# Optimization experiments

Hardware: AMD Instinct MI355X
Metric: run time of the kernel (lower is better)

Reference implementation:

```python
import jax, jax.numpy as jnp
import numpy as np

NS = 50000   # source nodes
NT = 50000   # target nodes
E = 500000   # edges per relation
H = 128      # hidden_channels
SF, TF, ED, OUT = 64, 48, 32, 2


def setup_inputs() -> dict:
    key = jax.random.key(0)
    ks = jax.random.split(key, 40)
    n = lambda i, shape, s=1.0: jax.random.normal(ks[i], shape, jnp.float32) * s
    W = 0.05  # weight scale
    inp = {
        'x_source': n(0, (NS, SF)),
        'x_target': n(1, (NT, TF)),
        'edge_attr_st': n(2, (E, ED)),
        'enc_s_w1': n(3, (H, SF), W), 'enc_s_b1': n(4, (H,), W),
        'enc_s_w2': n(5, (H, H), W), 'enc_s_b2': n(6, (H,), W),
        'enc_t_w1': n(7, (H, TF), W), 'enc_t_b1': n(8, (H,), W),
        'enc_t_w2': n(9, (H, H), W), 'enc_t_b2': n(10, (H,), W),
        'conv_wl': n(11, (3, 4, H, H), W),
        'conv_bl': n(12, (3, 4, H), W),
        'conv_wr': n(13, (3, 4, H, H), W),
        'gate_w1': n(14, (H, 2 * H), W), 'gate_b1': n(15, (H,), W),
        'gate_w2': n(16, (1, H), W), 'gate_b2': n(17, (1,), W),
        'mlp_w1': n(18, (H, H + ED), W), 'mlp_b1': n(19, (H,), W),
        'mlp_w2': n(20, (H // 2, H), W), 'mlp_b2': n(21, (H // 2,), W),
        'mlp_w3': n(22, (OUT, H // 2), W), 'mlp_b3': n(23, (OUT,), W),
        'ei_ss': jax.random.randint(ks[24], (2, E), 0, NS),
        'ei_tt': jax.random.randint(ks[25], (2, E), 0, NT),
        'ei_st': jax.random.randint(ks[26], (2, E), 0, NS),  # row<NS, col<NT (equal here)
        'ei_ts': jax.random.randint(ks[27], (2, E), 0, NT),
    }
    return inp


def _sage(x_src, x_dst, ei, wl, bl, wr, n_dst):
    # PyG SAGEConv(mean): lin_l(scatter_mean(x_src[row] -> col)) + lin_r(x_dst)
    row, col = ei[0], ei[1]
    msg = x_src[row]                                            # [E, H]
    s = jax.ops.segment_sum(msg, col, num_segments=n_dst)      # [n_dst, H]
    cnt = jax.ops.segment_sum(jnp.ones((ei.shape[1],), x_src.dtype), col,
                              num_segments=n_dst)
    agg = s / jnp.maximum(cnt, 1.0)[:, None]
    return agg @ wl.T + bl + x_dst @ wr.T


def reference(x_source, x_target, edge_attr_st,
              enc_s_w1, enc_s_b1, enc_s_w2, enc_s_b2,
              enc_t_w1, enc_t_b1, enc_t_w2, enc_t_b2,
              conv_wl, conv_bl, conv_wr,
              gate_w1, gate_b1, gate_w2, gate_b2,
              mlp_w1, mlp_b1, mlp_w2, mlp_b2, mlp_w3, mlp_b3,
              ei_ss, ei_tt, ei_st, ei_ts):
    relu = jax.nn.relu
    # node encoders (dropout is identity in eval)
    xs = relu(x_source @ enc_s_w1.T + enc_s_b1) @ enc_s_w2.T + enc_s_b2
    xt = relu(x_target @ enc_t_w1.T + enc_t_b1) @ enc_t_w2.T + enc_t_b2

    def hetero_layer(hs, ht, l):
        # relation order: 0=ss, 1=tt, 2=st, 3=ts
        o_ss = _sage(hs, hs, ei_ss, conv_wl[l, 0], conv_bl[l, 0], conv_wr[l, 0], NS)
        o_tt = _sage(ht, ht, ei_tt, conv_wl[l, 1], conv_bl[l, 1], conv_wr[l, 1], NT)
        o_st = _sage(hs, ht, ei_st, conv_wl[l, 2], conv_bl[l, 2], conv_wr[l, 2], NT)
        o_ts = _sage(ht, hs, ei_ts, conv_wl[l, 3], conv_bl[l, 3], conv_wr[l, 3], NS)
        # HeteroConv aggr='mean' over relations per destination node type
        return (o_ss + o_ts) * 0.5, (o_tt + o_st) * 0.5

    h1s, h1t = hetero_layer(xs, xt, 0)
    h1s, h1t = relu(h1s), relu(h1t)
    h2s, h2t = hetero_layer(h1s, h1t, 1)
    h2s, h2t = relu(h2s + h1s), relu(h2t + h1t)
    h3s, h3t = hetero_layer(h2s, h2t, 2)
    h3s, h3t = relu(h3s + h2s), relu(h3t + h2t)

    # edge head on ('source','to','target') — first non-empty relation
    row, col = ei_st[0], ei_st[1]
    src_h = h3s[row]                                            # [E, H]
    tgt_h = h3t[col]                                            # [E, H]
    cat = jnp.concatenate([src_h, tgt_h], axis=1)               # [E, 2H]
    gate = jax.nn.sigmoid(relu(cat @ gate_w1.T + gate_b1) @ gate_w2.T + gate_b2)
    combined = src_h * gate + tgt_h * (1.0 - gate)
    feat = jnp.concatenate([combined, edge_attr_st], axis=1)    # [E, H+ED]
    h = relu(feat @ mlp_w1.T + mlp_b1)
    h = relu(h @ mlp_w2.T + mlp_b2)
    return h @ mlp_w3.T + mlp_b3                                # [E, OUT]
```

## Files before the change

kernel.cpp:

```cpp
#include <hip/hip_runtime.h>
#include <cmath>

#define NSN 50000
#define NTN 50000
#define EE  500000
#define NBE ((size_t)NSN * 128)
#define NPASS 4
#define PRNG 12500

using short8 = __attribute__((ext_vector_type(8))) short;
using f32x4  = __attribute__((ext_vector_type(4))) float;
#define MFMA16(a, b, c) __builtin_amdgcn_mfma_f32_16x16x32_bf16(a, b, c, 0, 0, 0)

__device__ __forceinline__ float  b2f(ushort u) { return __uint_as_float(((uint)u) << 16); }
__device__ __forceinline__ ushort f2b(float f) {
  uint x = __float_as_uint(f);
  uint r = x + 0x7FFFu + ((x >> 16) & 1u);
  return (ushort)(r >> 16);
}
__device__ __forceinline__ float blo(uint x) { return __uint_as_float(x << 16); }
__device__ __forceinline__ float bhi(uint x) { return __uint_as_float(x & 0xFFFF0000u); }
__device__ __forceinline__ uint  pk2(float a, float b) { return (uint)f2b(a) | ((uint)f2b(b) << 16); }

__global__ void cvtall_k(const float* __restrict__ xs, const float* __restrict__ xt,
                         const float* __restrict__ wl,
                         const float* __restrict__ esw1, const float* __restrict__ esw2,
                         const float* __restrict__ etw1, const float* __restrict__ etw2,
                         ushort* __restrict__ xsB, ushort* __restrict__ xtB,
                         ushort* __restrict__ wlB, ushort* __restrict__ esw1B,
                         ushort* __restrict__ esw2B, ushort* __restrict__ etw1B,
                         ushort* __restrict__ etw2B) {
  int i = blockIdx.x * 256 + threadIdx.x;
  if (i < 3200000) { xsB[i] = f2b(xs[i]); return; }
  i -= 3200000;
  if (i < 3200000) {
    int r = i >> 6, k = i & 63;
    xtB[i] = (k < 48) ? f2b(xt[(size_t)r * 48 + k]) : (ushort)0;
    return;
  }
  i -= 3200000;
  if (i < 196608) { wlB[i] = f2b(wl[i]); return; }
  i -= 196608;
  if (i < 8192) { esw1B[i] = f2b(esw1[i]); return; }
  i -= 8192;
  if (i < 16384) { esw2B[i] = f2b(esw2[i]); return; }
  i -= 16384;
  if (i < 8192) {
    int r = i >> 6, k = i & 63;
    etw1B[i] = (k < 48) ? f2b(etw1[(size_t)r * 48 + k]) : (ushort)0;
    return;
  }
  i -= 8192;
  if (i < 16384) { etw2B[i] = f2b(etw2[i]); return; }
}

__global__ void wrc_k(const float* __restrict__ wr, const float* __restrict__ bl,
                      ushort* __restrict__ wrcB, float* __restrict__ blc) {
  int z = blockIdx.y;
  int l = z >> 1, dd = z & 1;
  int r1 = dd ? 1 : 0, r2 = dd ? 2 : 3;
  int idx = blockIdx.x * 256 + threadIdx.x;
  if (idx < 16384) {
    wrcB[(size_t)z * 16384 + idx] =
        f2b(wr[(size_t)(l * 4 + r1) * 16384 + idx] + wr[(size_t)(l * 4 + r2) * 16384 + idx]);
    if (idx < 128)
      blc[z * 128 + idx] = bl[(l * 4 + r1) * 128 + idx] + bl[(l * 4 + r2) * 128 + idx];
  }
}

__global__ void headw_k(const float* __restrict__ gw1, const float* __restrict__ mw1,
                        const float* __restrict__ mw2, const float* __restrict__ gb1,
                        const float* __restrict__ mb1,
                        ushort* __restrict__ Whead, float* __restrict__ biasHead,
                        ushort* __restrict__ w1eB, ushort* __restrict__ w2B) {
  int idx = blockIdx.x * 256 + threadIdx.x;
  if (idx < 65536) {
    int z = idx >> 15, rr = (idx >> 7) & 255, c = idx & 127;
    float v = (rr < 128) ? gw1[(size_t)rr * 256 + z * 128 + c]
                         : mw1[(size_t)(rr - 128) * 160 + c];
    Whead[idx] = f2b(v);
  } else if (idx < 69632) {
    int i = idx - 65536;
    w1eB[i] = f2b(mw1[(size_t)(i >> 5) * 160 + 128 + (i & 31)]);
  } else if (idx < 77824) {
    int i = idx - 69632;
    w2B[i] = f2b(mw2[i]);
  } else if (idx < 78336) {
    int i = idx - 77824;
    int z = i >> 8, n = i & 255;
    biasHead[i] = (n < 128) ? (z ? 0.f : gb1[n]) : mb1[n - 128];
  }
}

__global__ void count4_k(const int* __restrict__ e0, const int* __restrict__ e1,
                         const int* __restrict__ e2, const int* __restrict__ e3,
                         int* __restrict__ cnt) {
  int rel = blockIdx.y;
  const int* col = (rel == 0 ? e0 : rel == 1 ? e1 : rel == 2 ? e2 : e3) + EE;
  int i = blockIdx.x * 256 + threadIdx.x;
  if (i < EE) atomicAdd(&cnt[rel * 50000 + col[i]], 1);
}

__global__ __launch_bounds__(256) void scanA_k(const int* __restrict__ cnt,
                                               int* __restrict__ loc,
                                               int* __restrict__ bsum) {
  __shared__ int ws[4];
  int rel = blockIdx.y, b = blockIdx.x, t = threadIdx.x;
  const int* c = cnt + (size_t)rel * 50000;
  int base = b * 2048 + t * 8;
  int v[8], s = 0;
  #pragma unroll
  for (int i = 0; i < 8; ++i) {
    int idx = base + i;
    v[i] = (idx < 50000) ? c[idx] : 0;
    s += v[i];
  }
  int lane = t & 63, w = t >> 6;
  int x = s;
  #pragma unroll
  for (int d = 1; d < 64; d <<= 1) {
    int y = __shfl_up(x, d, 64);
    if (lane >= d) x += y;
  }
  if (lane == 63) ws[w] = x;
  __syncthreads();
  int add = 0;
  for (int ww = 0; ww < w; ++ww) add += ws[ww];
  int run = add + x - s;
  #pragma unroll
  for (int i = 0; i < 8; ++i) {
    int idx = base + i;
    run += v[i];
    if (idx < 50000) loc[(size_t)rel * 50000 + idx] = run;
  }
  if (t == 255) bsum[rel * 25 + b] = add + x;
}
__global__ void scanB_k(int* __restrict__ bsum) {
  int t = threadIdx.x;
  if (t < 4) {
    int s = 0;
    for (int b = 0; b < 25; ++b) {
      int v = bsum[t * 25 + b];
      bsum[t * 25 + b] = s;
      s += v;
    }
  }
}
__global__ void scanC_k(const int* __restrict__ cnt, int* __restrict__ loc,
                        const int* __restrict__ bsum, int* __restrict__ off,
                        int* __restrict__ cur) {
  int rel = blockIdx.y;
  int i = blockIdx.x * 256 + threadIdx.x;
  if (i < 50000) {
    int incl = loc[(size_t)rel * 50000 + i] + bsum[rel * 25 + i / 2048];
    off[(size_t)rel * 50001 + i + 1] = incl;
    cur[(size_t)rel * 50000 + i] = incl - cnt[(size_t)rel * 50000 + i];
    if (i == 0) off[(size_t)rel * 50001] = 0;
  }
}

__global__ void fillP_k(const int* __restrict__ e0, const int* __restrict__ e1,
                        const int* __restrict__ e2, const int* __restrict__ e3,
                        int* __restrict__ cur, int* __restrict__ adj,
                        int* __restrict__ adjE, int pass) {
  int rel = blockIdx.y;
  const int* ei = rel == 0 ? e0 : rel == 1 ? e1 : rel == 2 ? e2 : e3;
  int e = blockIdx.x * 256 + threadIdx.x;
  if (e < EE) {
    int c = ei[EE + e];
    if (c >= pass * PRNG && c < (pass + 1) * PRNG) {
      int pos = atomicAdd(&cur[rel * 50000 + c], 1);
      adj[(size_t)rel * EE + pos] = ei[e];
      if (rel == 2) adjE[pos] = e;
    }
  }
}

__global__ void colof_k(const int* __restrict__ off, int* __restrict__ colOf, int N) {
  int n = blockIdx.x * 256 + threadIdx.x;
  if (n < N) {
    int s = off[n], e = off[n + 1];
    for (int i = s; i < e; ++i) colOf[i] = n;
  }
}

__global__ void eaperm_k(const float* __restrict__ ea, const int* __restrict__ adjE,
                         ushort* __restrict__ eaB, int E) {
  int idx = blockIdx.x * 256 + threadIdx.x;
  int pos = idx >> 3, q = idx & 7;
  if (pos < E) {
    int eid = adjE[pos];
    float4 v = *(const float4*)(ea + (size_t)eid * 32 + q * 4);
    ushort4 o;
    o.x = f2b(v.x); o.y = f2b(v.y); o.z = f2b(v.z); o.w = f2b(v.w);
    *(ushort4*)(eaB + (size_t)pos * 32 + q * 4) = o;
  }
}

__global__ __launch_bounds__(256) void gather4_k(
    const ushort* __restrict__ hs, const ushort* __restrict__ ht,
    const int* __restrict__ off4, const int* __restrict__ adj4,
    ushort* __restrict__ m0, ushort* __restrict__ m1,
    ushort* __restrict__ m2, ushort* __restrict__ m3, int N) {
  int r = blockIdx.y;
  const ushort* src = (r == 0 || r == 2) ? hs : ht;
  ushort* dst = r == 0 ? m0 : (r == 1 ? m1 : (r == 2 ? m2 : m3));
  const int* off = off4 + r * 50001;
  const int* adj = adj4 + (size_t)r * EE;
  int t = threadIdx.x;
  int n = blockIdx.x * 4 + (t >> 6);
  if (n >= N) return;
  int lane = t & 63, g = lane >> 4, i = lane & 15;
  int s = off[n], e = off[n + 1];
  float a[8] = {};
  int k = s + g;
  for (; k + 4 < e; k += 8) {
    int r0 = adj[k], r1 = adj[k + 4];
    uint4 v0 = *(const uint4*)(src + (size_t)r0 * 128 + i * 8);
    uint4 v1 = *(const uint4*)(src + (size_t)r1 * 128 + i * 8);
    a[0] += blo(v0.x) + blo(v1.x); a[1] += bhi(v0.x) + bhi(v1.x);
    a[2] += blo(v0.y) + blo(v1.y); a[3] += bhi(v0.y) + bhi(v1.y);
    a[4] += blo(v0.z) + blo(v1.z); a[5] += bhi(v0.z) + bhi(v1.z);
    a[6] += blo(v0.w) + blo(v1.w); a[7] += bhi(v0.w) + bhi(v1.w);
  }
  if (k < e) {
    int r0 = adj[k];
    uint4 v = *(const uint4*)(src + (size_t)r0 * 128 + i * 8);
    a[0] += blo(v.x); a[1] += bhi(v.x);
    a[2] += blo(v.y); a[3] += bhi(v.y);
    a[4] += blo(v.z); a[5] += bhi(v.z);
    a[6] += blo(v.w); a[7] += bhi(v.w);
  }
  #pragma unroll
  for (int c = 0; c < 8; ++c) {
    a[c] += __shfl_xor(a[c], 16, 64);
    a[c] += __shfl_xor(a[c], 32, 64);
  }
  if (g == 0) {
    float inv = 1.f / (float)max(e - s, 1);
    uint4 o;
    o.x = pk2(a[0] * inv, a[1] * inv);
    o.y = pk2(a[2] * inv, a[3] * inv);
    o.z = pk2(a[4] * inv, a[5] * inv);
    o.w = pk2(a[6] * inv, a[7] * inv);
    *(uint4*)(dst + (size_t)n * 128 + i * 8) = o;
  }
}

template <int MODE>
__device__ __forceinline__ void gemm_body(
    ushort (*As)[40], ushort (*Ws)[40],
    const ushort* __restrict__ A, const ushort* __restrict__ W,
    const float* __restrict__ bias, ushort* __restrict__ C,
    int M, int K, int ldc, int m0) {
  int t = threadIdx.x;
  int lane = t & 63, w = t >> 6, wm = w >> 1, wn = w & 1;
  f32x4 zz = {0.f, 0.f, 0.f, 0.f};
  f32x4 acc[4][4];
  #pragma unroll
  for (int i = 0; i < 4; ++i)
    #pragma unroll
    for (int j = 0; j < 4; ++j) acc[i][j] = zz;
  for (int kb = 0; kb < K; kb += 32) {
    #pragma unroll
    for (int s = 0; s < 2; ++s) {
      int idx = t + s * 256;
      int r = idx >> 2, c = idx & 3;
      int gm = m0 + r;
      uint4 va = make_uint4(0, 0, 0, 0);
      if (gm < M) va = *(const uint4*)(A + (size_t)gm * K + kb + c * 8);
      *(uint4*)&As[r][c * 8] = va;
      *(uint4*)&Ws[r][c * 8] = *(const uint4*)(W + (size_t)r * K + kb + c * 8);
    }
    __syncthreads();
    short8 af[4], bf[4];
    #pragma unroll
    for (int mf = 0; mf < 4; ++mf)
      af[mf] = *(const short8*)&As[wm * 64 + mf * 16 + (lane & 15)][(lane >> 4) * 8];
    #pragma unroll
    for (int nf = 0; nf < 4; ++nf)
      bf[nf] = *(const short8*)&Ws[wn * 64 + nf * 16 + (lane & 15)][(lane >> 4) * 8];
    #pragma unroll
    for (int mf = 0; mf < 4; ++mf)
      #pragma unroll
      for (int nf = 0; nf < 4; ++nf) acc[mf][nf] = MFMA16(af[mf], bf[nf], acc[mf][nf]);
    __syncthreads();
  }
  int r0 = (lane >> 4) * 4, nin = lane & 15;
  #pragma unroll
  for (int mf = 0; mf < 4; ++mf)
    #pragma unroll
    for (int nf = 0; nf < 4; ++nf) {
      int n = wn * 64 + nf * 16 + nin;
      float bv = bias ? bias[n] : 0.f;
      #pragma unroll
      for (int i = 0; i < 4; ++i) {
        int gm = m0 + wm * 64 + mf * 16 + r0 + i;
        if (gm >= M) continue;
        float v = acc[mf][nf][i] + bv;
        if (MODE == 1) v = fmaxf(v, 0.f);
        C[(size_t)gm * ldc + n] = f2b(v);
      }
    }
}

template <int MODE>
__global__ __launch_bounds__(256) void enc_k(
    const ushort* A0, const ushort* A1, const ushort* W0, const ushort* W1,
    const float* b0, const float* b1, ushort* C0, ushort* C1, int M, int K) {
  __shared__ alignas(16) ushort As[128][40];
  __shared__ alignas(16) ushort Ws[128][40];
  int y = blockIdx.y;
  gemm_body<MODE>(As, Ws, y ? A1 : A0, y ? W1 : W0, y ? b1 : b0, y ? C1 : C0,
                  M, K, 128, blockIdx.x * 128);
}

__global__ __launch_bounds__(256) void gemmH_k(
    const ushort* Abase, const ushort* Whead, const float* biasHead,
    ushort* pS, ushort* pT) {
  __shared__ alignas(16) ushort As[128][40];
  __shared__ alignas(16) ushort Ws[128][40];
  int z = blockIdx.z, ny = blockIdx.y;
  gemm_body<0>(As, Ws, Abase + (size_t)z * NBE,
               Whead + ((size_t)z * 256 + ny * 128) * 128,
               biasHead + z * 256 + ny * 128,
               (z ? pT : pS) + ny * 128,
               NSN, 128, 256, blockIdx.x * 128);
}

template <int RES>
__global__ __launch_bounds__(256) void lgemm_k(
    const ushort* __restrict__ hs, const ushort* __restrict__ ht,
    const ushort* __restrict__ m0, const ushort* __restrict__ m1,
    const ushort* __restrict__ m2, const ushort* __restrict__ m3,
    const ushort* __restrict__ wlL, const ushort* __restrict__ wrcL,
    const float* __restrict__ blcL,
    ushort* __restrict__ hsOut, ushort* __restrict__ htOut, int M) {
  __shared__ alignas(16) ushort As[128][40];
  __shared__ alignas(16) ushort Ws[128][40];
  int t = threadIdx.x;
  int y = blockIdx.y;
  int m0i = blockIdx.x * 128;
  const ushort* A0 = y ? m1 : m0;
  const ushort* A1 = y ? m2 : m3;
  const ushort* self = y ? ht : hs;
  const ushort* W0 = wlL + (size_t)(y ? 1 : 0) * 16384;
  const ushort* W1 = wlL + (size_t)(y ? 2 : 3) * 16384;
  const ushort* W2 = wrcL + (size_t)y * 16384;
  const float* bias = blcL + y * 128;
  ushort* C = y ? htOut : hsOut;

  int lane = t & 63, w = t >> 6, wm = w >> 1, wn = w & 1;
  f32x4 zz = {0.f, 0.f, 0.f, 0.f};
  f32x4 acc[4][4];
  #pragma unroll
  for (int i = 0; i < 4; ++i)
    #pragma unroll
    for (int j = 0; j < 4; ++j) acc[i][j] = zz;
  for (int p = 0; p < 3; ++p) {
    const ushort* A = p == 0 ? A0 : (p == 1 ? A1 : self);
    const ushort* Wp = p == 0 ? W0 : (p == 1 ? W1 : W2);
    for (int kb = 0; kb < 128; kb += 32) {
      #pragma unroll
      for (int s = 0; s < 2; ++s) {
        int idx = t + s * 256;
        int r = idx >> 2, c = idx & 3;
        int gm = m0i + r;
        uint4 va = make_uint4(0, 0, 0, 0);
        if (gm < M) va = *(const uint4*)(A + (size_t)gm * 128 + kb + c * 8);
        *(uint4*)&As[r][c * 8] = va;
        *(uint4*)&Ws[r][c * 8] = *(const uint4*)(Wp + (size_t)r * 128 + kb + c * 8);
      }
      __syncthreads();
      short8 af[4], bf[4];
      #pragma unroll
      for (int mf = 0; mf < 4; ++mf)
        af[mf] = *(const short8*)&As[wm * 64 + mf * 16 + (lane & 15)][(lane >> 4) * 8];
      #pragma unroll
      for (int nf = 0; nf < 4; ++nf)
        bf[nf] = *(const short8*)&Ws[wn * 64 + nf * 16 + (lane & 15)][(lane >> 4) * 8];
      #pragma unroll
      for (int mf = 0; mf < 4; ++mf)
        #pragma unroll
        for (int nf = 0; nf < 4; ++nf) acc[mf][nf] = MFMA16(af[mf], bf[nf], acc[mf][nf]);
      __syncthreads();
    }
  }
  int r0 = (lane >> 4) * 4, nin = lane & 15;
  #pragma unroll
  for (int mf = 0; mf < 4; ++mf)
    #pragma unroll
    for (int nf = 0; nf < 4; ++nf) {
      int n = wn * 64 + nf * 16 + nin;
      float bv = bias[n];
      #pragma unroll
      for (int i = 0; i < 4; ++i) {
        int gm = m0i + wm * 64 + mf * 16 + r0 + i;
        if (gm >= M) continue;
        float v = 0.5f * (acc[mf][nf][i] + bv);
        if (RES) v += b2f(self[(size_t)gm * 128 + n]);
        C[(size_t)gm * 128 + n] = f2b(fmaxf(v, 0.f));
      }
    }
}

__global__ __launch_bounds__(256) void head_k(
    const ushort* __restrict__ pS, const ushort* __restrict__ pT,
    const int* __restrict__ erowA, const int* __restrict__ ecolA,
    const int* __restrict__ eidA, const ushort* __restrict__ eaB,
    const ushort* __restrict__ w1eB, const ushort* __restrict__ w2B,
    const float* __restrict__ gw2, const float* __restrict__ gb2p,
    const float* __restrict__ mb2, const float* __restrict__ mw3,
    const float* __restrict__ mb3, float* __restrict__ out, int E) {
  __shared__ alignas(16) ushort h1s[64][136];
  __shared__ int er[64], ec[64], eidS[64];
  __shared__ alignas(16) float gw2s[128];
  __shared__ alignas(16) float mw3s[128];
  __shared__ float mb2s[64];
  float (*h2F)[68] = (float(*)[68])&h1s[0][0];

  int nwg = gridDim.x;
  int bid = blockIdx.x;
  int q = nwg >> 3, r = nwg & 7;
  int xcd = bid & 7, sub = bid >> 3;
  int swz = (xcd < r ? xcd * (q + 1) : r * (q + 1) + (xcd - r) * q) + sub;
  int e0 = swz * 64;

  int t = threadIdx.x;
  if (t < 64) {
    int p = e0 + t;
    er[t] = (p < E) ? erowA[p] : 0;
    eidS[t] = (p < E) ? eidA[p] : -1;
    mb2s[t] = mb2[t];
  } else if (t < 128) {
    int p = e0 + (t - 64);
    ec[t - 64] = (p < E) ? ecolA[p] : 0;
  }
  if (t < 128) gw2s[t] = gw2[t];
  else mw3s[t - 128] = mw3[t - 128];
  __syncthreads();
  int lane = t & 63, w = t >> 6;
  {
    int p = e0 + w * 16 + (lane & 15);
    short8 a = {};
    if (p < E) a = *(const short8*)(eaB + (size_t)p * 32 + (lane >> 4) * 8);
    int ebase = w * 16 + (lane >> 4) * 4;
    #pragma unroll
    for (int nf = 0; nf < 8; ++nf) {
      short8 b = *(const short8*)(w1eB + (size_t)(nf * 16 + (lane & 15)) * 32 + (lane >> 4) * 8);
      f32x4 cz = {0.f, 0.f, 0.f, 0.f};
      cz = MFMA16(a, b, cz);
      int jj = nf * 16 + (lane & 15);
      #pragma unroll
      for (int i = 0; i < 4; ++i) h1s[ebase + i][jj] = f2b(cz[i]);
    }
  }
  __syncthreads();
  {
    int el = lane >> 2, qq = lane & 3, e = w * 16 + el;
    int j0 = qq * 32;
    const ushort* ps = pS + (size_t)er[e] * 256;
    const ushort* pt = pT + (size_t)ec[e] * 256;
    float dot = 0.f;
    #pragma unroll
    for (int cc = 0; cc < 4; ++cc) {
      int j = j0 + cc * 8;
      uint4 ga = *(const uint4*)(ps + j);
      uint4 gb = *(const uint4*)(pt + j);
      const float* gp = &gw2s[j];
      float h;
      h = fmaxf(blo(ga.x) + blo(gb.x), 0.f); dot = fmaf(h, gp[0], dot);
      h = fmaxf(bhi(ga.x) + bhi(gb.x), 0.f); dot = fmaf(h, gp[1], dot);
      h = fmaxf(blo(ga.y) + blo(gb.y), 0.f); dot = fmaf(h, gp[2], dot);
      h = fmaxf(bhi(ga.y) + bhi(gb.y), 0.f); dot = fmaf(h, gp[3], dot);
      h = fmaxf(blo(ga.z) + blo(gb.z), 0.f); dot = fmaf(h, gp[4], dot);
      h = fmaxf(bhi(ga.z) + bhi(gb.z), 0.f); dot = fmaf(h, gp[5], dot);
      h = fmaxf(blo(ga.w) + blo(gb.w), 0.f); dot = fmaf(h, gp[6], dot);
      h = fmaxf(bhi(ga.w) + bhi(gb.w), 0.f); dot = fmaf(h, gp[7], dot);
    }
    dot += __shfl_xor(dot, 1, 64);
    dot += __shfl_xor(dot, 2, 64);
    float g = 1.f / (1.f + __expf(-(dot + gb2p[0])));
    float om = 1.f - g;
    #pragma unroll
    for (int cc = 0; cc < 4; ++cc) {
      int j = j0 + cc * 8;
      uint4 uu = *(const uint4*)(ps + 128 + j);
      uint4 vv = *(const uint4*)(pt + 128 + j);
      uint4 ee = *(const uint4*)&h1s[e][j];
      uint o0 = pk2(fmaxf(fmaf(g, blo(uu.x), om * blo(vv.x)) + blo(ee.x), 0.f),
                    fmaxf(fmaf(g, bhi(uu.x), om * bhi(vv.x)) + bhi(ee.x), 0.f));
      uint o1 = pk2(fmaxf(fmaf(g, blo(uu.y), om * blo(vv.y)) + blo(ee.y), 0.f),
                    fmaxf(fmaf(g, bhi(uu.y), om * bhi(vv.y)) + bhi(ee.y), 0.f));
      uint o2 = pk2(fmaxf(fmaf(g, blo(uu.z), om * blo(vv.z)) + blo(ee.z), 0.f),
                    fmaxf(fmaf(g, bhi(uu.z), om * bhi(vv.z)) + bhi(ee.z), 0.f));
      uint o3 = pk2(fmaxf(fmaf(g, blo(uu.w), om * blo(vv.w)) + blo(ee.w), 0.f),
                    fmaxf(fmaf(g, bhi(uu.w), om * bhi(vv.w)) + bhi(ee.w), 0.f));
      *(uint4*)&h1s[e][j] = make_uint4(o0, o1, o2, o3);
    }
  }
  __syncthreads();
  {
    f32x4 zz = {0.f, 0.f, 0.f, 0.f};
    f32x4 acc[4] = {zz, zz, zz, zz};
    #pragma unroll
    for (int ks = 0; ks < 4; ++ks) {
      short8 a = *(const short8*)&h1s[w * 16 + (lane & 15)][ks * 32 + (lane >> 4) * 8];
      #pragma unroll
      for (int nf = 0; nf < 4; ++nf) {
        short8 b = *(const short8*)(w2B + (size_t)(nf * 16 + (lane & 15)) * 128 + ks * 32 + (lane >> 4) * 8);
        acc[nf] = MFMA16(a, b, acc[nf]);
      }
    }
    __syncthreads();
    int ebase = w * 16 + (lane >> 4) * 4;
    #pragma unroll
    for (int nf = 0; nf < 4; ++nf) {
      int n = nf * 16 + (lane & 15);
      #pragma unroll
      for (int i = 0; i < 4; ++i)
        h2F[ebase + i][n] = fmaxf(acc[nf][i] + mb2s[n], 0.f);
    }
  }
  __syncthreads();
  if (t < 128) {
    int e = t >> 1, o = t & 1;
    int eid = eidS[e];
    if (eid >= 0) {
      float s = mb3[o];
      #pragma unroll
      for (int kk = 0; kk < 64; kk += 4) {
        float4 hv = *(const float4*)&h2F[e][kk];
        float4 wv = *(const float4*)&mw3s[o * 64 + kk];
        s = fmaf(hv.x, wv.x, s); s = fmaf(hv.y, wv.y, s);
        s = fmaf(hv.z, wv.z, s); s = fmaf(hv.w, wv.w, s);
      }
      out[(size_t)eid * 2 + o] = s;
    }
  }
}

extern "C" void kernel_launch(void* const* d_in, const int* in_sizes, int n_in,
                              void* d_out, int out_size, void* d_ws, size_t ws_size,
                              hipStream_t stream) {
  const float* x_source = (const float*)d_in[0];
  const float* x_target = (const float*)d_in[1];
  const float* edge_attr = (const float*)d_in[2];
  const float* enc_s_w1 = (const float*)d_in[3];
  const float* enc_s_b1 = (const float*)d_in[4];
  const float* enc_s_w2 = (const float*)d_in[5];
  const float* enc_s_b2 = (const float*)d_in[6];
  const float* enc_t_w1 = (const float*)d_in[7];
  const float* enc_t_b1 = (const float*)d_in[8];
  const float* enc_t_w2 = (const float*)d_in[9];
  const float* enc_t_b2 = (const float*)d_in[10];
  const float* conv_wl = (const float*)d_in[11];
  const float* conv_bl = (const float*)d_in[12];
  const float* conv_wr = (const float*)d_in[13];
  const float* gate_w1 = (const float*)d_in[14];
  const float* gate_b1 = (const float*)d_in[15];
  const float* gate_w2 = (const float*)d_in[16];
  const float* gate_b2 = (const float*)d_in[17];
  const float* mlp_w1 = (const float*)d_in[18];
  const float* mlp_b1 = (const float*)d_in[19];
  const float* mlp_w2 = (const float*)d_in[20];
  const float* mlp_b2 = (const float*)d_in[21];
  const float* mlp_w3 = (const float*)d_in[22];
  const float* mlp_b3 = (const float*)d_in[23];
  const int* ei[4] = {(const int*)d_in[24], (const int*)d_in[25],
                      (const int*)d_in[26], (const int*)d_in[27]};
  float* out = (float*)d_out;

  char* wsp = (char*)d_ws;
  size_t off = 0;
  auto alloc = [&](size_t bytes) {
    char* p = wsp + off;
    off += (bytes + 255) & ~(size_t)255;
    return p;
  };
  ushort* nbase = (ushort*)alloc(4 * NBE * 2);
  ushort* nb[4];
  for (int i = 0; i < 4; ++i) nb[i] = nbase + (size_t)i * NBE;
  ushort* shared4 = (ushort*)alloc(4 * NBE * 2);
  ushort* mB[4];
  for (int i = 0; i < 4; ++i) mB[i] = shared4 + (size_t)i * NBE;
  int* adj4 = (int*)alloc((size_t)4 * EE * 4);
  int* off4 = (int*)alloc(4 * 50001 * 4);
  int* cur4 = (int*)alloc(4 * 50000 * 4);
  int* cnt4 = (int*)alloc(4 * 50000 * 4);
  int* bsum = (int*)alloc(128 * 4);
  ushort* xsB = (ushort*)alloc((size_t)NSN * 64 * 2);
  ushort* xtB = (ushort*)alloc((size_t)NTN * 64 * 2);
  ushort* esw1B = (ushort*)alloc(128 * 64 * 2);
  ushort* esw2B = (ushort*)alloc(128 * 128 * 2);
  ushort* etw1B = (ushort*)alloc(128 * 64 * 2);
  ushort* etw2B = (ushort*)alloc(128 * 128 * 2);
  ushort* wlB = (ushort*)alloc((size_t)12 * 16384 * 2);
  ushort* wrcB = (ushort*)alloc((size_t)6 * 16384 * 2);
  float* blc = (float*)alloc(6 * 128 * 4);
  ushort* Whead = (ushort*)alloc((size_t)2 * 256 * 128 * 2);
  float* biasHead = (float*)alloc(2 * 256 * 4);
  ushort* w1eB = (ushort*)alloc(128 * 32 * 2);
  ushort* w2B = (ushort*)alloc(64 * 128 * 2);

  cvtall_k<<<(6645760 + 255) / 256, 256, 0, stream>>>(
      x_source, x_target, conv_wl, enc_s_w1, enc_s_w2, enc_t_w1, enc_t_w2,
      xsB, xtB, wlB, esw1B, esw2B, etw1B, etw2B);
  wrc_k<<<dim3(64, 6), 256, 0, stream>>>(conv_wr, conv_bl, wrcB, blc);
  headw_k<<<307, 256, 0, stream>>>(gate_w1, mlp_w1, mlp_w2, gate_b1, mlp_b1,
                                   Whead, biasHead, w1eB, w2B);
  int gm = (NSN + 127) / 128;
  enc_k<1><<<dim3(gm, 2), 256, 0, stream>>>(xsB, xtB, esw1B, etw1B,
      enc_s_b1, enc_t_b1, nb[2], nb[3], NSN, 64);
  enc_k<0><<<dim3(gm, 2), 256, 0, stream>>>(nb[2], nb[3], esw2B, etw2B,
      enc_s_b2, enc_t_b2, nb[0], nb[1], NSN, 128);

  int* adjE = (int*)xsB;
  int* colOf = (int*)xtB;
  hipMemsetAsync(cnt4, 0, 4 * 50000 * sizeof(int), stream);
  int cb = (EE + 255) / 256;
  count4_k<<<dim3(cb, 4), 256, 0, stream>>>(ei[0], ei[1], ei[2], ei[3], cnt4);
  scanA_k<<<dim3(25, 4), 256, 0, stream>>>(cnt4, cur4, bsum);
  scanB_k<<<1, 64, 0, stream>>>(bsum);
  scanC_k<<<dim3((50000 + 255) / 256, 4), 256, 0, stream>>>(cnt4, cur4, bsum, off4, cur4);
  for (int p = 0; p < NPASS; ++p)
    fillP_k<<<dim3(cb, 4), 256, 0, stream>>>(ei[0], ei[1], ei[2], ei[3], cur4, adj4, adjE, p);
  colof_k<<<(50000 + 255) / 256, 256, 0, stream>>>(off4 + 2 * 50001, colOf, NTN);

  int gb = (NSN + 3) / 4;
  {
    gather4_k<<<dim3(gb, 4), 256, 0, stream>>>(nb[0], nb[1], off4, adj4,
        mB[0], mB[1], mB[2], mB[3], NSN);
    lgemm_k<0><<<dim3(gm, 2), 256, 0, stream>>>(nb[0], nb[1],
        mB[0], mB[1], mB[2], mB[3], wlB, wrcB, blc, nb[2], nb[3], NSN);
    gather4_k<<<dim3(gb, 4), 256, 0, stream>>>(nb[2], nb[3], off4, adj4,
        mB[0], mB[1], mB[2], mB[3], NSN);
    lgemm_k<1><<<dim3(gm, 2), 256, 0, stream>>>(nb[2], nb[3],
        mB[0], mB[1], mB[2], mB[3], wlB + (size_t)4 * 16384,
        wrcB + (size_t)2 * 16384, blc + 256, nb[0], nb[1], NSN);
    gather4_k<<<dim3(gb, 4), 256, 0, stream>>>(nb[0], nb[1], off4, adj4,
        mB[0], mB[1], mB[2], mB[3], NSN);
    lgemm_k<1><<<dim3(gm, 2), 256, 0, stream>>>(nb[0], nb[1],
        mB[0], mB[1], mB[2], mB[3], wlB + (size_t)8 * 16384,
        wrcB + (size_t)4 * 16384, blc + 512, nb[2], nb[3], NSN);
  }

  ushort* pS = shared4;
  ushort* pT = shared4 + 2 * NBE;
  gemmH_k<<<dim3(gm, 2, 2), 256, 0, stream>>>(nbase + 2 * NBE, Whead, biasHead, pS, pT);

  ushort* eaB = nbase;
  eaperm_k<<<((EE * 8) + 255) / 256, 256, 0, stream>>>(edge_attr, adjE, eaB, EE);

  head_k<<<(EE + 63) / 64, 256, 0, stream>>>(pS, pT,
      adj4 + (size_t)2 * EE, colOf, adjE, eaB, w1eB, w2B,
      gate_w2, gate_b2, mlp_b2, mlp_w3, mlp_b3, out, EE);
}
```

Before: 821.1 us.

## Fuse encoder GEMMs, fold colOf into scan, halve fill passes, hoist loads

The two encoder linear layers are merged into one kernel that keeps the ReLU hidden activations in shared memory instead of writing them to global memory and reading them back. The colOf fill is folded into the final scan kernel for relation 2, and the fill kernel's destination-range pass count drops from 4 to 2. In the edge-head kernel, all gathered pS/pT loads are issued up front so their memory latency overlaps. The aim is fewer launches and less global traffic. The costs are more shared memory and registers per block, which may reduce occupancy, and wider-range fill passes that may hurt scatter locality.

```diff
diff --git a/kernel.cpp b/kernel.cpp
--- a/kernel.cpp
+++ b/kernel.cpp
@@ -5,8 +5,8 @@
 #define NTN 50000
 #define EE  500000
 #define NBE ((size_t)NSN * 128)
-#define NPASS 4
-#define PRNG 12500
+#define NPASS 2
+#define PRNG 25000
 
 using short8 = __attribute__((ext_vector_type(8))) short;
 using f32x4  = __attribute__((ext_vector_type(4))) float;
@@ -146,16 +146,20 @@
     }
   }
 }
-__global__ void scanC_k(const int* __restrict__ cnt, int* __restrict__ loc,
+__global__ void scanC_k(const int* __restrict__ cnt, const int* __restrict__ loc,
                         const int* __restrict__ bsum, int* __restrict__ off,
-                        int* __restrict__ cur) {
+                        int* __restrict__ cur, int* __restrict__ colOf) {
   int rel = blockIdx.y;
   int i = blockIdx.x * 256 + threadIdx.x;
   if (i < 50000) {
     int incl = loc[(size_t)rel * 50000 + i] + bsum[rel * 25 + i / 2048];
+    int cntv = cnt[(size_t)rel * 50000 + i];
     off[(size_t)rel * 50001 + i + 1] = incl;
-    cur[(size_t)rel * 50000 + i] = incl - cnt[(size_t)rel * 50000 + i];
+    cur[(size_t)rel * 50000 + i] = incl - cntv;
     if (i == 0) off[(size_t)rel * 50001] = 0;
+    if (rel == 2) {
+      for (int k = incl - cntv; k < incl; ++k) colOf[k] = i;
+    }
   }
 }
 
@@ -173,14 +177,6 @@
       adj[(size_t)rel * EE + pos] = ei[e];
       if (rel == 2) adjE[pos] = e;
     }
-  }
-}
-
-__global__ void colof_k(const int* __restrict__ off, int* __restrict__ colOf, int N) {
-  int n = blockIdx.x * 256 + threadIdx.x;
-  if (n < N) {
-    int s = off[n], e = off[n + 1];
-    for (int i = s; i < e; ++i) colOf[i] = n;
   }
 }
 
@@ -304,15 +300,112 @@
     }
 }
 
-template <int MODE>
-__global__ __launch_bounds__(256) void enc_k(
-    const ushort* A0, const ushort* A1, const ushort* W0, const ushort* W1,
-    const float* b0, const float* b1, ushort* C0, ushort* C1, int M, int K) {
+__global__ __launch_bounds__(256) void encf_k(
+    const ushort* __restrict__ A0, const ushort* __restrict__ A1,
+    const ushort* __restrict__ W10, const ushort* __restrict__ W11,
+    const ushort* __restrict__ W20, const ushort* __restrict__ W21,
+    const float* __restrict__ b10, const float* __restrict__ b11,
+    const float* __restrict__ b20, const float* __restrict__ b21,
+    ushort* __restrict__ C0, ushort* __restrict__ C1, int M) {
   __shared__ alignas(16) ushort As[128][40];
   __shared__ alignas(16) ushort Ws[128][40];
+  __shared__ alignas(16) ushort H1[128][136];
   int y = blockIdx.y;
-  gemm_body<MODE>(As, Ws, y ? A1 : A0, y ? W1 : W0, y ? b1 : b0, y ? C1 : C0,
-                  M, K, 128, blockIdx.x * 128);
+  const ushort* A  = y ? A1 : A0;
+  const ushort* W1 = y ? W11 : W10;
+  const ushort* W2 = y ? W21 : W20;
+  const float* b1 = y ? b11 : b10;
+  const float* b2 = y ? b21 : b20;
+  ushort* C = y ? C1 : C0;
+  int t = threadIdx.x;
+  int m0 = blockIdx.x * 128;
+  int lane = t & 63, w = t >> 6, wm = w >> 1, wn = w & 1;
+  f32x4 zz = {0.f, 0.f, 0.f, 0.f};
+  f32x4 acc[4][4];
+  #pragma unroll
+  for (int i = 0; i < 4; ++i)
+    #pragma unroll
+    for (int j = 0; j < 4; ++j) acc[i][j] = zz;
+  for (int kb = 0; kb < 64; kb += 32) {
+    #pragma unroll
+    for (int s = 0; s < 2; ++s) {
+      int idx = t + s * 256;
+      int r = idx >> 2, c = idx & 3;
+      int gm = m0 + r;
+      uint4 va = make_uint4(0, 0, 0, 0);
+      if (gm < M) va = *(const uint4*)(A + (size_t)gm * 64 + kb + c * 8);
+      *(uint4*)&As[r][c * 8] = va;
+      *(uint4*)&Ws[r][c * 8] = *(const uint4*)(W1 + (size_t)r * 64 + kb + c * 8);
+    }
+    __syncthreads();
+    short8 af[4], bf[4];
+    #pragma unroll
+    for (int mf = 0; mf < 4; ++mf)
+      af[mf] = *(const short8*)&As[wm * 64 + mf * 16 + (lane & 15)][(lane >> 4) * 8];
+    #pragma unroll
+    for (int nf = 0; nf < 4; ++nf)
+      bf[nf] = *(const short8*)&Ws[wn * 64 + nf * 16 + (lane & 15)][(lane >> 4) * 8];
+    #pragma unroll
+    for (int mf = 0; mf < 4; ++mf)
+      #pragma unroll
+      for (int nf = 0; nf < 4; ++nf) acc[mf][nf] = MFMA16(af[mf], bf[nf], acc[mf][nf]);
+    __syncthreads();
+  }
+  {
+    int r0 = (lane >> 4) * 4, nin = lane & 15;
+    #pragma unroll
+    for (int mf = 0; mf < 4; ++mf)
+      #pragma unroll
+      for (int nf = 0; nf < 4; ++nf) {
+        int n = wn * 64 + nf * 16 + nin;
+        float bv = b1[n];
+        #pragma unroll
+        for (int i = 0; i < 4; ++i)
+          H1[wm * 64 + mf * 16 + r0 + i][n] = f2b(fmaxf(acc[mf][nf][i] + bv, 0.f));
+      }
+  }
+  __syncthreads();
+  #pragma unroll
+  for (int i = 0; i < 4; ++i)
+    #pragma unroll
+    for (int j = 0; j < 4; ++j) acc[i][j] = zz;
+  for (int kb = 0; kb < 128; kb += 32) {
+    #pragma unroll
+    for (int s = 0; s < 2; ++s) {
+      int idx = t + s * 256;
+      int r = idx >> 2, c = idx & 3;
+      *(uint4*)&Ws[r][c * 8] = *(const uint4*)(W2 + (size_t)r * 128 + kb + c * 8);
+    }
+    __syncthreads();
+    short8 af[4], bf[4];
+    #pragma unroll
+    for (int mf = 0; mf < 4; ++mf)
+      af[mf] = *(const short8*)&H1[wm * 64 + mf * 16 + (lane & 15)][kb + (lane >> 4) * 8];
+    #pragma unroll
+    for (int nf = 0; nf < 4; ++nf)
+      bf[nf] = *(const short8*)&Ws[wn * 64 + nf * 16 + (lane & 15)][(lane >> 4) * 8];
+    #pragma unroll
+    for (int mf = 0; mf < 4; ++mf)
+      #pragma unroll
+      for (int nf = 0; nf < 4; ++nf) acc[mf][nf] = MFMA16(af[mf], bf[nf], acc[mf][nf]);
+    __syncthreads();
+  }
+  {
+    int r0 = (lane >> 4) * 4, nin = lane & 15;
+    #pragma unroll
+    for (int mf = 0; mf < 4; ++mf)
+      #pragma unroll
+      for (int nf = 0; nf < 4; ++nf) {
+        int n = wn * 64 + nf * 16 + nin;
+        float bv = b2[n];
+        #pragma unroll
+        for (int i = 0; i < 4; ++i) {
+          int gm = m0 + wm * 64 + mf * 16 + r0 + i;
+          if (gm >= M) continue;
+          C[(size_t)gm * 128 + n] = f2b(acc[mf][nf][i] + bv);
+        }
+      }
+  }
 }
 
 __global__ __launch_bounds__(256) void gemmH_k(
@@ -461,22 +554,28 @@
     int j0 = qq * 32;
     const ushort* ps = pS + (size_t)er[e] * 256;
     const ushort* pt = pT + (size_t)ec[e] * 256;
-    float dot = 0.f;
+    uint4 ga[4], gb[4], uu[4], vv[4];
     #pragma unroll
     for (int cc = 0; cc < 4; ++cc) {
       int j = j0 + cc * 8;
-      uint4 ga = *(const uint4*)(ps + j);
-      uint4 gb = *(const uint4*)(pt + j);
-      const float* gp = &gw2s[j];
+      ga[cc] = *(const uint4*)(ps + j);
+      gb[cc] = *(const uint4*)(pt + j);
+      uu[cc] = *(const uint4*)(ps + 128 + j);
+      vv[cc] = *(const uint4*)(pt + 128 + j);
+    }
+    float dot = 0.f;
+    #pragma unroll
+    for (int cc = 0; cc < 4; ++cc) {
+      const float* gp = &gw2s[j0 + cc * 8];
       float h;
-      h = fmaxf(blo(ga.x) + blo(gb.x), 0.f); dot = fmaf(h, gp[0], dot);
-      h = fmaxf(bhi(ga.x) + bhi(gb.x), 0.f); dot = fmaf(h, gp[1], dot);
-      h = fmaxf(blo(ga.y) + blo(gb.y), 0.f); dot = fmaf(h, gp[2], dot);
-      h = fmaxf(bhi(ga.y) + bhi(gb.y), 0.f); dot = fmaf(h, gp[3], dot);
-      h = fmaxf(blo(ga.z) + blo(gb.z), 0.f); dot = fmaf(h, gp[4], dot);
-      h = fmaxf(bhi(ga.z) + bhi(gb.z), 0.f); dot = fmaf(h, gp[5], dot);
-      h = fmaxf(blo(ga.w) + blo(gb.w), 0.f); dot = fmaf(h, gp[6], dot);
-      h = fmaxf(bhi(ga.w) + bhi(gb.w), 0.f); dot = fmaf(h, gp[7], dot);
+      h = fmaxf(blo(ga[cc].x) + blo(gb[cc].x), 0.f); dot = fmaf(h, gp[0], dot);
+      h = fmaxf(bhi(ga[cc].x) + bhi(gb[cc].x), 0.f); dot = fmaf(h, gp[1], dot);
+      h = fmaxf(blo(ga[cc].y) + blo(gb[cc].y), 0.f); dot = fmaf(h, gp[2], dot);
+      h = fmaxf(bhi(ga[cc].y) + bhi(gb[cc].y), 0.f); dot = fmaf(h, gp[3], dot);
+      h = fmaxf(blo(ga[cc].z) + blo(gb[cc].z), 0.f); dot = fmaf(h, gp[4], dot);
+      h = fmaxf(bhi(ga[cc].z) + bhi(gb[cc].z), 0.f); dot = fmaf(h, gp[5], dot);
+      h = fmaxf(blo(ga[cc].w) + blo(gb[cc].w), 0.f); dot = fmaf(h, gp[6], dot);
+      h = fmaxf(bhi(ga[cc].w) + bhi(gb[cc].w), 0.f); dot = fmaf(h, gp[7], dot);
     }
     dot += __shfl_xor(dot, 1, 64);
     dot += __shfl_xor(dot, 2, 64);
@@ -485,17 +584,15 @@
     #pragma unroll
     for (int cc = 0; cc < 4; ++cc) {
       int j = j0 + cc * 8;
-      uint4 uu = *(const uint4*)(ps + 128 + j);
-      uint4 vv = *(const uint4*)(pt + 128 + j);
       uint4 ee = *(const uint4*)&h1s[e][j];
-      uint o0 = pk2(fmaxf(fmaf(g, blo(uu.x), om * blo(vv.x)) + blo(ee.x), 0.f),
-                    fmaxf(fmaf(g, bhi(uu.x), om * bhi(vv.x)) + bhi(ee.x), 0.f));
-      uint o1 = pk2(fmaxf(fmaf(g, blo(uu.y), om * blo(vv.y)) + blo(ee.y), 0.f),
-                    fmaxf(fmaf(g, bhi(uu.y), om * bhi(vv.y)) + bhi(ee.y), 0.f));
-      uint o2 = pk2(fmaxf(fmaf(g, blo(uu.z), om * blo(vv.z)) + blo(ee.z), 0.f),
-                    fmaxf(fmaf(g, bhi(uu.z), om * bhi(vv.z)) + bhi(ee.z), 0.f));
-      uint o3 = pk2(fmaxf(fmaf(g, blo(uu.w), om * blo(vv.w)) + blo(ee.w), 0.f),
-                    fmaxf(fmaf(g, bhi(uu.w), om * bhi(vv.w)) + bhi(ee.w), 0.f));
+      uint o0 = pk2(fmaxf(fmaf(g, blo(uu[cc].x), om * blo(vv[cc].x)) + blo(ee.x), 0.f),
+                    fmaxf(fmaf(g, bhi(uu[cc].x), om * bhi(vv[cc].x)) + bhi(ee.x), 0.f));
+      uint o1 = pk2(fmaxf(fmaf(g, blo(uu[cc].y), om * blo(vv[cc].y)) + blo(ee.y), 0.f),
+                    fmaxf(fmaf(g, bhi(uu[cc].y), om * bhi(vv[cc].y)) + bhi(ee.y), 0.f));
+      uint o2 = pk2(fmaxf(fmaf(g, blo(uu[cc].z), om * blo(vv[cc].z)) + blo(ee.z), 0.f),
+                    fmaxf(fmaf(g, bhi(uu[cc].z), om * bhi(vv[cc].z)) + bhi(ee.z), 0.f));
+      uint o3 = pk2(fmaxf(fmaf(g, blo(uu[cc].w), om * blo(vv[cc].w)) + blo(ee.w), 0.f),
+                    fmaxf(fmaf(g, bhi(uu[cc].w), om * bhi(vv[cc].w)) + bhi(ee.w), 0.f));
       *(uint4*)&h1s[e][j] = make_uint4(o0, o1, o2, o3);
     }
   }
@@ -610,10 +707,8 @@
   headw_k<<<307, 256, 0, stream>>>(gate_w1, mlp_w1, mlp_w2, gate_b1, mlp_b1,
                                    Whead, biasHead, w1eB, w2B);
   int gm = (NSN + 127) / 128;
-  enc_k<1><<<dim3(gm, 2), 256, 0, stream>>>(xsB, xtB, esw1B, etw1B,
-      enc_s_b1, enc_t_b1, nb[2], nb[3], NSN, 64);
-  enc_k<0><<<dim3(gm, 2), 256, 0, stream>>>(nb[2], nb[3], esw2B, etw2B,
-      enc_s_b2, enc_t_b2, nb[0], nb[1], NSN, 128);
+  encf_k<<<dim3(gm, 2), 256, 0, stream>>>(xsB, xtB, esw1B, etw1B, esw2B, etw2B,
+      enc_s_b1, enc_t_b1, enc_s_b2, enc_t_b2, nb[0], nb[1], NSN);
 
   int* adjE = (int*)xsB;
   int* colOf = (int*)xtB;
@@ -622,10 +717,10 @@
   count4_k<<<dim3(cb, 4), 256, 0, stream>>>(ei[0], ei[1], ei[2], ei[3], cnt4);
   scanA_k<<<dim3(25, 4), 256, 0, stream>>>(cnt4, cur4, bsum);
   scanB_k<<<1, 64, 0, stream>>>(bsum);
-  scanC_k<<<dim3((50000 + 255) / 256, 4), 256, 0, stream>>>(cnt4, cur4, bsum, off4, cur4);
+  scanC_k<<<dim3((50000 + 255) / 256, 4), 256, 0, stream>>>(cnt4, cur4, bsum, off4,
+                                                            cur4, colOf);
   for (int p = 0; p < NPASS; ++p)
     fillP_k<<<dim3(cb, 4), 256, 0, stream>>>(ei[0], ei[1], ei[2], ei[3], cur4, adj4, adjE, p);
-  colof_k<<<(50000 + 255) / 256, 256, 0, stream>>>(off4 + 2 * 50001, colOf, NTN);
 
   int gb = (NSN + 3) / 4;
   {
```

Measured after the change: 790.0 us. 3.8% less time.
